# Performance work log

Measured on AMD Instinct MI355X. Metric: run time of the kernel, lower is better.

Reference implementation:

```python
import jax, jax.numpy as jnp
import numpy as np

K_SIZE = 5  # kernel_size=[5]


def setup_inputs() -> dict:
    key = jax.random.key(0)
    k1, k2 = jax.random.split(key)
    bs, N, h, w, c = 4, 8, 256, 256, 1
    frames = jax.random.normal(k1, (bs, N, h, w, c), dtype=jnp.float32)
    core = jax.random.normal(k2, (bs, h, w, N * K_SIZE * K_SIZE * c), dtype=jnp.float32)
    return {"frames": frames, "core": core}


def _kpn_filter(frames, core):
    # frames: (bs, N, h, w, c); core: (bs, h, w, N*K*K*c)
    bs, N, h, w, c = frames.shape
    K = K_SIZE
    # _convert_dict: raw reshape of core to (bs, N, h, w, c, K*K)
    core_r = jnp.reshape(core, (bs, N, h, w, c, K * K))
    p = K // 2
    fpad = jnp.pad(frames, ((0, 0), (0, 0), (p, p), (p, p), (0, 0)))
    # K*K shifted views stacked on last axis: (bs, N, h, w, c, K*K)
    img_stack = jnp.stack(
        [fpad[:, :, i:i + h, j:j + w, :] for i in range(K) for j in range(K)],
        axis=-1,
    )
    # per-pixel dynamic-kernel weighted sum
    pred_img_i = jnp.sum(core_r * img_stack, axis=-1)  # (bs, N, h, w, c)
    # single kernel size -> mean over kernel axis is identity
    pred_img = jnp.mean(pred_img_i, axis=1)  # (bs, h, w, c), mean over burst N
    return pred_img, pred_img_i


def reference(frames, core):
    return _kpn_filter(frames, core)
```

## Files before the change

### kernel.cpp

```cpp
#include <hip/hip_runtime.h>

#define H 256
#define W 256

typedef float f4 __attribute__((ext_vector_type(4)));

__global__ __launch_bounds__(256, 4)
void kpn_fused(const float* __restrict__ frames, const float* __restrict__ core,
               float* __restrict__ pred, float* __restrict__ pred_i) {
  __shared__ f4 smem[8 * 5 * 34];
  __shared__ f4 red[256];

  const int tid = threadIdx.x;
  const int bid = blockIdx.x;
  const int blk = (bid & 7) * 256 + (bid >> 3);
  const int xh  = blk & 1;
  const int y   = (blk >> 1) & 255;
  const int b   = blk >> 9;

  const int n = tid >> 5;
  const int q = tid & 31;

  const int g = ((b * 8 + n) * 256 + y) * 64 + xh * 32 + q;
  const f4* c4 = (const f4*)(core + (size_t)g * 100);
  f4 wv[25];
#pragma unroll
  for (int k = 0; k < 25; ++k) {
    wv[k] = c4[k];
  }
  __builtin_amdgcn_sched_barrier(0);

  for (int i = tid; i < 8 * 5 * 34; i += 256) {
    const int nn  = i / 170;
    const int rem = i - nn * 170;
    const int r   = rem / 34;
    const int c   = rem - r * 34;
    const int yy  = y + r - 2;
    const int x4  = xh * 128 + (c - 1) * 4;
    f4 v = {0.f, 0.f, 0.f, 0.f};
    if ((unsigned)yy < (unsigned)H && (unsigned)x4 <= 252u) {
      v = *(const f4*)(frames + ((size_t)(b * 8 + nn) * H + yy) * W + x4);
    }
    smem[i] = v;
  }
#pragma unroll
  for (int k = 0; k < 25; ++k) {
    asm volatile("" : "+v"(wv[k]));
  }
  __syncthreads();

  f4 acc = {0.f, 0.f, 0.f, 0.f};
#pragma unroll
  for (int ki = 0; ki < 5; ++ki) {
    const f4* row = &smem[(n * 5 + ki) * 34 + q];
    f4 a0 = row[0], a1 = row[1], a2 = row[2];
    float fr[12] = {a0[0], a0[1], a0[2], a0[3],
                    a1[0], a1[1], a1[2], a1[3],
                    a2[0], a2[1], a2[2], a2[3]};
#pragma unroll
    for (int kj = 0; kj < 5; ++kj) {
#pragma unroll
      for (int p = 0; p < 4; ++p) {
        const int f = p * 25 + ki * 5 + kj;
        acc[p] += wv[f >> 2][f & 3] * fr[p + kj + 2];
      }
    }
  }

  red[tid] = acc;
  __syncthreads();
  if (tid < 32) {
    f4 s = {0.f, 0.f, 0.f, 0.f};
#pragma unroll
    for (int k = 0; k < 8; ++k) {
      s += red[tid + 32 * k];
    }
    s *= 0.125f;
    __builtin_nontemporal_store(
        s, (f4*)(pred + ((size_t)b * 256 + y) * 256 + xh * 128 + tid * 4));
  }

  __builtin_nontemporal_store(acc, (f4*)(pred_i + (size_t)g * 4));
}

extern "C" void kernel_launch(void* const* d_in, const int* in_sizes, int n_in,
                              void* d_out, int out_size, void* d_ws, size_t ws_size,
                              hipStream_t stream) {
  const float* frames = (const float*)d_in[0];
  const float* core   = (const float*)d_in[1];
  float* pred   = (float*)d_out;
  float* pred_i = pred + (size_t)4 * H * W;

  hipLaunchKernelGGL(kpn_fused, dim3(2048), dim3(256), 0, stream,
                     frames, core, pred, pred_i);
}
```

Baseline: 39.21 us.

## Split each 4-pixel group's 100 weights across a quad of threads

Measured after the change: 37.40 us (median of 2 runs). 4.6% less time.

```diff
diff --git a/kernel.cpp b/kernel.cpp
--- a/kernel.cpp
+++ b/kernel.cpp
@@ -6,37 +6,39 @@
 typedef float f4 __attribute__((ext_vector_type(4)));
 
 __global__ __launch_bounds__(256, 4)
-void kpn_fused(const float* __restrict__ frames, const float* __restrict__ core,
-               float* __restrict__ pred, float* __restrict__ pred_i) {
-  __shared__ f4 smem[8 * 5 * 34];
-  __shared__ f4 red[256];
+void kpn_quad(const float* __restrict__ frames, const float* __restrict__ core,
+              float* __restrict__ pred, float* __restrict__ pred_i) {
+  __shared__ f4 smem[8 * 5 * 10];
+  __shared__ f4 red[64];
 
   const int tid = threadIdx.x;
   const int bid = blockIdx.x;
-  const int blk = (bid & 7) * 256 + (bid >> 3);
-  const int xh  = blk & 1;
-  const int y   = (blk >> 1) & 255;
-  const int b   = blk >> 9;
+  const int blk = (bid & 7) * 1024 + (bid >> 3);
+  const int xq  = blk & 7;
+  const int y   = (blk >> 3) & 255;
+  const int b   = blk >> 11;
 
   const int n = tid >> 5;
-  const int q = tid & 31;
+  const int q = (tid >> 2) & 7;
+  const int j = tid & 3;
 
-  const int g = ((b * 8 + n) * 256 + y) * 64 + xh * 32 + q;
+  const int g = ((b * 8 + n) * 256 + y) * 64 + xq * 8 + q;
   const f4* c4 = (const f4*)(core + (size_t)g * 100);
-  f4 wv[25];
+  f4 wv[7];
 #pragma unroll
-  for (int k = 0; k < 25; ++k) {
-    wv[k] = c4[k];
+  for (int m = 0; m < 6; ++m) {
+    wv[m] = c4[4 * m + j];
   }
+  wv[6] = c4[24];
   __builtin_amdgcn_sched_barrier(0);
 
-  for (int i = tid; i < 8 * 5 * 34; i += 256) {
-    const int nn  = i / 170;
-    const int rem = i - nn * 170;
-    const int r   = rem / 34;
-    const int c   = rem - r * 34;
+  for (int i = tid; i < 400; i += 256) {
+    const int nn  = i / 50;
+    const int rem = i - nn * 50;
+    const int r   = rem / 10;
+    const int c   = rem - r * 10;
     const int yy  = y + r - 2;
-    const int x4  = xh * 128 + (c - 1) * 4;
+    const int x4  = xq * 32 + (c - 1) * 4;
     f4 v = {0.f, 0.f, 0.f, 0.f};
     if ((unsigned)yy < (unsigned)H && (unsigned)x4 <= 252u) {
       v = *(const f4*)(frames + ((size_t)(b * 8 + nn) * H + yy) * W + x4);
@@ -44,43 +46,56 @@
     smem[i] = v;
   }
 #pragma unroll
-  for (int k = 0; k < 25; ++k) {
-    asm volatile("" : "+v"(wv[k]));
+  for (int m = 0; m < 7; ++m) {
+    asm volatile("" : "+v"(wv[m]));
   }
   __syncthreads();
 
-  f4 acc = {0.f, 0.f, 0.f, 0.f};
+  f4 w4[5][3];
 #pragma unroll
   for (int ki = 0; ki < 5; ++ki) {
-    const f4* row = &smem[(n * 5 + ki) * 34 + q];
-    f4 a0 = row[0], a1 = row[1], a2 = row[2];
-    float fr[12] = {a0[0], a0[1], a0[2], a0[3],
-                    a1[0], a1[1], a1[2], a1[3],
-                    a2[0], a2[1], a2[2], a2[3]};
-#pragma unroll
-    for (int kj = 0; kj < 5; ++kj) {
-#pragma unroll
-      for (int p = 0; p < 4; ++p) {
-        const int f = p * 25 + ki * 5 + kj;
-        acc[p] += wv[f >> 2][f & 3] * fr[p + kj + 2];
-      }
-    }
+    const f4* row = &smem[(n * 5 + ki) * 10 + q];
+    w4[ki][0] = row[0]; w4[ki][1] = row[1]; w4[ki][2] = row[2];
   }
 
-  red[tid] = acc;
+  f4 acc = {0.f, 0.f, 0.f, 0.f};
+#define DO_F(J, M, E)                                                     \
+  { constexpr int f  = 16 * (M) + 4 * (J) + (E);                          \
+    constexpr int p  = f / 25, kd = f % 25;                               \
+    constexpr int ki = kd / 5, kj = kd % 5, wx = p + kj + 2;              \
+    acc[p] += wv[M][E] * w4[ki][wx >> 2][wx & 3]; }
+#define DO4(J, M) DO_F(J, M, 0) DO_F(J, M, 1) DO_F(J, M, 2) DO_F(J, M, 3)
+  switch (j) {
+    case 0: DO4(0,0) DO4(0,1) DO4(0,2) DO4(0,3) DO4(0,4) DO4(0,5) DO4(0,6) break;
+    case 1: DO4(1,0) DO4(1,1) DO4(1,2) DO4(1,3) DO4(1,4) DO4(1,5) break;
+    case 2: DO4(2,0) DO4(2,1) DO4(2,2) DO4(2,3) DO4(2,4) DO4(2,5) break;
+    default:DO4(3,0) DO4(3,1) DO4(3,2) DO4(3,3) DO4(3,4) DO4(3,5) break;
+  }
+#undef DO4
+#undef DO_F
+
+#pragma unroll
+  for (int c = 0; c < 4; ++c) {
+    acc[c] += __shfl_xor(acc[c], 1, 64);
+    acc[c] += __shfl_xor(acc[c], 2, 64);
+  }
+
+  if (j == 0) red[tid >> 2] = acc;
   __syncthreads();
   if (tid < 32) {
-    f4 s = {0.f, 0.f, 0.f, 0.f};
+    const int qq = tid >> 2, p = tid & 3;
+    float s = 0.f;
 #pragma unroll
     for (int k = 0; k < 8; ++k) {
-      s += red[tid + 32 * k];
+      s += red[k * 8 + qq][p];
     }
     s *= 0.125f;
     __builtin_nontemporal_store(
-        s, (f4*)(pred + ((size_t)b * 256 + y) * 256 + xh * 128 + tid * 4));
+        s, pred + ((size_t)b * 256 + y) * 256 + xq * 32 + tid);
   }
 
-  __builtin_nontemporal_store(acc, (f4*)(pred_i + (size_t)g * 4));
+  float out = (j == 0) ? acc[0] : (j == 1) ? acc[1] : (j == 2) ? acc[2] : acc[3];
+  __builtin_nontemporal_store(out, pred_i + (size_t)g * 4 + j);
 }
 
 extern "C" void kernel_launch(void* const* d_in, const int* in_sizes, int n_in,
@@ -91,6 +106,6 @@
   float* pred   = (float*)d_out;
   float* pred_i = pred + (size_t)4 * H * W;
 
-  hipLaunchKernelGGL(kpn_fused, dim3(2048), dim3(256), 0, stream,
+  hipLaunchKernelGGL(kpn_quad, dim3(8192), dim3(256), 0, stream,
                      frames, core, pred, pred_i);
 }
```
